# Kernel optimization log

Hardware: AMD Instinct MI355X
Metric: run time of the kernel (lower is better)

## Reference

```python
import jax, jax.numpy as jnp
import numpy as np

N_E = 8192
E_DIM = 512
BETA = 0.25


def setup_inputs() -> dict:
    key = jax.random.key(0)
    k1, k2, k3, k4 = jax.random.split(key, 4)
    x = jax.random.normal(k1, (32, 512, E_DIM), dtype=jnp.float32)
    label = jax.random.randint(k2, (32, 512), 0, 100, dtype=jnp.int64)
    idx = jax.random.randint(k3, (32, 512), 0, 512, dtype=jnp.int64)
    # codebook initialized uniform(-1/n_e, 1/n_e) as in the torch module
    W = jax.random.uniform(k4, (N_E, E_DIM), dtype=jnp.float32,
                           minval=-1.0 / N_E, maxval=1.0 / N_E)
    return {"x": x, "label": label, "idx": idx, "W": W}


def reference(x, label, idx, W):
    # label/idx are unused in the forward math (mirrors the torch module)
    latent = x.reshape(-1, E_DIM)                        # [N, e_dim]
    # squared euclidean distances: ||z||^2 + ||c||^2 - 2 z c^T
    d = (jnp.sum(latent ** 2, axis=1, keepdims=True)
         + jnp.sum(W ** 2, axis=1)[None, :]
         - 2.0 * jnp.matmul(latent, W.T))                # [N, n_e]
    indices = jnp.argmin(d, axis=-1)                     # [N]
    x_q = W[indices].reshape(x.shape)                    # gather + reshape
    commitment_loss = jnp.mean((jax.lax.stop_gradient(x_q) - x) ** 2)
    loss = BETA * commitment_loss
    # straight-through estimator
    x_q = x + jax.lax.stop_gradient(x_q - x)
    indices = indices.reshape(x.shape[:-1])
    return x_q, loss, indices
```

## Files before the change

### kernel.cpp

```cpp
#include <hip/hip_runtime.h>
#include <cstdint>
#include <cstddef>

#define EDIM  512
#define NROWS 16384
#define NE    8192
#define XQSZ  (NROWS * EDIM)
#define NTILE 64
#define K3    1536

#define OFF_PART  0
#define OFF_Z     16384
#define OFF_C2    81920
#define OFF_KEYS  114688
#define OFF_TMIN  245760
#define OFF_CNT   4440064
#define OFF_LIST  4441088
#define OFF_XE    8635392
#define OFF_WE    58967040

typedef __attribute__((ext_vector_type(8)))  short          short8;
typedef __attribute__((ext_vector_type(16))) float          f32x16;
typedef __attribute__((ext_vector_type(4)))  unsigned short u16x4;

__global__ void k_rownorm(const float* __restrict__ in, float* __restrict__ out, int nrows) {
#pragma clang fp contract(off)
    int row = blockIdx.x * blockDim.x + threadIdx.x;
    if (row >= nrows) return;
    const float* p = in + (size_t)row * EDIM;
    float S[4];
#pragma unroll
    for (int b = 0; b < 4; ++b) {
        const float* q = p + b * 128;
        float r[8];
#pragma unroll
        for (int j = 0; j < 8; ++j) { float v = q[j]; r[j] = v * v; }
        for (int i = 8; i < 128; i += 8) {
#pragma unroll
            for (int j = 0; j < 8; ++j) { float v = q[i + j]; r[j] = r[j] + v * v; }
        }
        S[b] = ((r[0] + r[1]) + (r[2] + r[3])) + ((r[4] + r[5]) + (r[6] + r[7]));
    }
    out[row] = (S[0] + S[1]) + (S[2] + S[3]);
}

__device__ __forceinline__ unsigned short f2bf(float f) {
    unsigned u = __float_as_uint(f);
    return (unsigned short)((u + 0x7FFFu + ((u >> 16) & 1u)) >> 16);
}
__device__ __forceinline__ float bf2f(unsigned short h) {
    return __uint_as_float(((unsigned)h) << 16);
}

__global__ __launch_bounds__(256) void k_split3(const float* __restrict__ in,
        unsigned short* __restrict__ outp, int nrows) {
    int e = blockIdx.x * 256 + threadIdx.x;
    int row = e >> 7;
    int d0  = (e & 127) << 2;
    if (row >= nrows) return;
    float4 v = *(const float4*)(in + (size_t)row * EDIM + d0);
    float vv[4] = {v.x, v.y, v.z, v.w};
    u16x4 H, M, L;
#pragma unroll
    for (int i = 0; i < 4; ++i) {
        float f = vv[i];
        unsigned short h = f2bf(f);
        float r1 = f - bf2f(h);
        unsigned short m = f2bf(r1);
        float r2 = r1 - bf2f(m);
        L[i] = f2bf(r2); H[i] = h; M[i] = m;
    }
    unsigned short* o = outp + (size_t)row * K3 + d0;
    *(u16x4*)(o) = H; *(u16x4*)(o + EDIM) = M; *(u16x4*)(o + 2 * EDIM) = L;
}

__device__ __forceinline__ void gld16(const void* g, void* l) {
    __builtin_amdgcn_global_load_lds((const __attribute__((address_space(1))) void*)g,
                                     (__attribute__((address_space(3))) void*)l, 16, 0, 0);
}

#define GBM 128
#define GBN 128
#define GBK 64

__global__ __launch_bounds__(256) void k_argmin_hi(
        const unsigned short* __restrict__ Xe, const unsigned short* __restrict__ We,
        const float* __restrict__ c2, unsigned* __restrict__ tmin) {
    __shared__ __align__(16) unsigned short At[GBM * GBK];
    __shared__ __align__(16) unsigned short Bt[GBN * GBK];
    __shared__ unsigned smin[GBM];

    const int tid = threadIdx.x;
    const int lane = tid & 63, wid = tid >> 6;
    const int wr = wid >> 1, wc = wid & 1;

    const int bid = blockIdx.x;
    const int swz = (bid & 7) * 1024 + (bid >> 3);
    const int rowtile = swz & 127, codetile = swz >> 7;
    const int row0 = rowtile * GBM, code0 = codetile * GBN;

    if (tid < GBM) smin[tid] = 0xFFFFFFFFu;

    f32x16 acc[2][2];
#pragma unroll
    for (int i = 0; i < 2; ++i)
#pragma unroll
        for (int j = 0; j < 2; ++j)
#pragma unroll
            for (int r = 0; r < 16; ++r) acc[i][j][r] = 0.0f;

    size_t ga[4], gb[4];
#pragma unroll
    for (int i = 0; i < 4; ++i) {
        int chunk = i * 256 + tid;
        int row   = chunk >> 3;
        int kcs   = (chunk & 7) ^ (row & 7);
        ga[i] = (size_t)(row0 + row) * K3 + kcs * 8;
        gb[i] = (size_t)(code0 + row) * K3 + kcs * 8;
    }

    const int ra0 = wr * 64 + (lane & 31);
    const int rb0 = wc * 64 + (lane & 31);
    const int kh  = lane >> 5;
    const int sa  = ra0 & 7, sb = rb0 & 7;

    for (int kt = 0; kt < EDIM / GBK; ++kt) {
        const size_t ko = (size_t)kt * GBK;
#pragma unroll
        for (int i = 0; i < 4; ++i) {
            gld16(Xe + ga[i] + ko, (char*)At + i * 4096 + wid * 1024);
            gld16(We + gb[i] + ko, (char*)Bt + i * 4096 + wid * 1024);
        }
        __syncthreads();
#pragma unroll
        for (int ks = 0; ks < 4; ++ks) {
            const int ch = ks * 2 + kh;
            short8 a0 = *(const short8*)((const char*)At + ra0 * 128        + ((ch ^ sa) * 16));
            short8 a1 = *(const short8*)((const char*)At + (ra0 + 32) * 128 + ((ch ^ sa) * 16));
            short8 b0 = *(const short8*)((const char*)Bt + rb0 * 128        + ((ch ^ sb) * 16));
            short8 b1 = *(const short8*)((const char*)Bt + (rb0 + 32) * 128 + ((ch ^ sb) * 16));
            acc[0][0] = __builtin_amdgcn_mfma_f32_32x32x16_bf16(a0, b0, acc[0][0], 0, 0, 0);
            acc[0][1] = __builtin_amdgcn_mfma_f32_32x32x16_bf16(a0, b1, acc[0][1], 0, 0, 0);
            acc[1][0] = __builtin_amdgcn_mfma_f32_32x32x16_bf16(a1, b0, acc[1][0], 0, 0, 0);
            acc[1][1] = __builtin_amdgcn_mfma_f32_32x32x16_bf16(a1, b1, acc[1][1], 0, 0, 0);
        }
        __syncthreads();
    }

    const int j0 = code0 + wc * 64 + (lane & 31);
    const float c20 = c2[j0], c21 = c2[j0 + 32];
#pragma unroll
    for (int mi = 0; mi < 2; ++mi) {
#pragma unroll
        for (int reg = 0; reg < 16; ++reg) {
            const int rl = wr * 64 + mi * 32 + (reg & 3) + 8 * (reg >> 2) + 4 * kh;
            const float d0 = (4.0f + c20) - 2.0f * acc[mi][0][reg];
            const float d1 = (4.0f + c21) - 2.0f * acc[mi][1][reg];
            unsigned u0 = __float_as_uint(d0), u1 = __float_as_uint(d1);
            unsigned u = u0 < u1 ? u0 : u1;
#pragma unroll
            for (int m = 1; m <= 16; m <<= 1) {
                unsigned o = __shfl_xor(u, m, 64);
                if (o < u) u = o;
            }
            if ((lane & 31) == 0) atomicMin(&smin[rl], u);
        }
    }
    __syncthreads();
    if (tid < GBM) tmin[codetile * NROWS + row0 + tid] = smin[tid];
}

__global__ __launch_bounds__(256) void k_select(
        const unsigned* __restrict__ tmin, const float* __restrict__ Z,
        int* __restrict__ cnt, int* __restrict__ list) {
    const int row = blockIdx.x * 256 + threadIdx.x;
    unsigned mn = 0xFFFFFFFFu;
    for (int t = 0; t < NTILE; ++t) {
        unsigned v = tmin[t * NROWS + row];
        if (v < mn) mn = v;
    }
    const float margin = 4.35e-5f * sqrtf(Z[row]) + 1.7e-4f;
    const float thr = __uint_as_float(mn) + margin;
    for (int t = 0; t < NTILE; ++t) {
        if (__uint_as_float(tmin[t * NROWS + row]) <= thr) {
            int p = atomicAdd(&cnt[t], 1);
            list[t * NROWS + p] = row;
        }
    }
}

__global__ __launch_bounds__(256) void k_rescore_mfma(
        const unsigned short* __restrict__ Xe, const unsigned short* __restrict__ We,
        const float* __restrict__ Z, const float* __restrict__ c2,
        const int* __restrict__ cnt, const int* __restrict__ list,
        unsigned long long* __restrict__ keys) {
    __shared__ __align__(16) unsigned short At[GBM * GBK];
    __shared__ __align__(16) unsigned short Bt[GBN * GBK];
    __shared__ int rl_s[GBM];
    __shared__ float Zs[GBM];

    const int tile = blockIdx.x;
    const int n = cnt[tile];
    if (n == 0) return;
    const int* rows = list + tile * NROWS;
    const int tid = threadIdx.x;
    const int lane = tid & 63, wid = tid >> 6;
    const int wr = wid >> 1, wc = wid & 1;
    const int code0 = tile * 128;

    const int ra0 = wr * 64 + (lane & 31);
    const int rb0 = wc * 64 + (lane & 31);
    const int kh  = lane >> 5;
    const int sa  = ra0 & 7, sb = rb0 & 7;
    const int j0 = code0 + wc * 64 + (lane & 31);
    const float c20 = c2[j0], c21 = c2[j0 + 32];

    for (int chk = (int)blockIdx.y; chk * GBM < n; chk += 16) {
        __syncthreads();
        if (tid < GBM) {
            int ri = chk * GBM + tid;
            int r = rows[ri < n ? ri : 0];
            rl_s[tid] = r;
            Zs[tid] = Z[r];
        }
        __syncthreads();

        size_t aoff[4], boff[4];
#pragma unroll
        for (int i = 0; i < 4; ++i) {
            int chunk = i * 256 + tid;
            int row   = chunk >> 3;
            int kcs   = (chunk & 7) ^ (row & 7);
            aoff[i] = (size_t)rl_s[row] * K3 + kcs * 8;
            boff[i] = (size_t)(code0 + row) * K3 + kcs * 8;
        }

        f32x16 acc[2][2];
#pragma unroll
        for (int i = 0; i < 2; ++i)
#pragma unroll
            for (int j = 0; j < 2; ++j)
#pragma unroll
                for (int r = 0; r < 16; ++r) acc[i][j][r] = 0.0f;

#pragma unroll
        for (int bt = 0; bt < 6; ++bt) {
            const int ao = (bt == 1 || bt == 2) ? EDIM : (bt == 4 ? 2 * EDIM : 0);
            const int bo = (bt == 0 || bt == 2) ? EDIM : (bt == 3 ? 2 * EDIM : 0);
            for (int kc = 0; kc < 8; ++kc) {
                const int ko = ao + kc * GBK;
                const int kob = bo + kc * GBK;
#pragma unroll
                for (int i = 0; i < 4; ++i) {
                    gld16(Xe + aoff[i] + ko,  (char*)At + i * 4096 + wid * 1024);
                    gld16(We + boff[i] + kob, (char*)Bt + i * 4096 + wid * 1024);
                }
                __syncthreads();
#pragma unroll
                for (int ks = 0; ks < 4; ++ks) {
                    const int ch = ks * 2 + kh;
                    short8 a0 = *(const short8*)((const char*)At + ra0 * 128        + ((ch ^ sa) * 16));
                    short8 a1 = *(const short8*)((const char*)At + (ra0 + 32) * 128 + ((ch ^ sa) * 16));
                    short8 b0 = *(const short8*)((const char*)Bt + rb0 * 128        + ((ch ^ sb) * 16));
                    short8 b1 = *(const short8*)((const char*)Bt + (rb0 + 32) * 128 + ((ch ^ sb) * 16));
                    acc[0][0] = __builtin_amdgcn_mfma_f32_32x32x16_bf16(a0, b0, acc[0][0], 0, 0, 0);
                    acc[0][1] = __builtin_amdgcn_mfma_f32_32x32x16_bf16(a0, b1, acc[0][1], 0, 0, 0);
                    acc[1][0] = __builtin_amdgcn_mfma_f32_32x32x16_bf16(a1, b0, acc[1][0], 0, 0, 0);
                    acc[1][1] = __builtin_amdgcn_mfma_f32_32x32x16_bf16(a1, b1, acc[1][1], 0, 0, 0);
                }
                __syncthreads();
            }
        }

#pragma unroll
        for (int mi = 0; mi < 2; ++mi) {
#pragma unroll
            for (int reg = 0; reg < 16; ++reg) {
                const int rl = wr * 64 + mi * 32 + (reg & 3) + 8 * (reg >> 2) + 4 * kh;
                const float Zr = Zs[rl];
                const float d0 = (Zr + c20) - 2.0f * acc[mi][0][reg];
                const float d1 = (Zr + c21) - 2.0f * acc[mi][1][reg];
                unsigned long long k0 = (((unsigned long long)__float_as_uint(d0)) << 13) | (unsigned)j0;
                unsigned long long k1 = (((unsigned long long)__float_as_uint(d1)) << 13) | (unsigned)(j0 + 32);
                unsigned long long k = k0 < k1 ? k0 : k1;
#pragma unroll
                for (int m = 1; m <= 16; m <<= 1) {
                    unsigned long long o = __shfl_xor(k, m, 64);
                    if (o < k) k = o;
                }
                if ((lane & 31) == 0) atomicMin(&keys[rl_s[rl]], k);
            }
        }
    }
}

__global__ __launch_bounds__(256) void k_gather(
        const float* __restrict__ x, const float* __restrict__ W,
        const unsigned long long* __restrict__ keys,
        float* __restrict__ out, double* __restrict__ part) {
    const int tid = threadIdx.x;
    const int row = blockIdx.x * 8 + (tid >> 5);
    const int c = tid & 31;
    const int idx = (int)(keys[row] & 0x1FFFull);

    const float* wrow = W + (size_t)idx * EDIM;
    const float* xrow = x + (size_t)row * EDIM;
    float* orow = out + (size_t)row * EDIM;

    double lsum = 0.0;
#pragma unroll
    for (int v = 0; v < 4; ++v) {
        const int d = c * 4 + v * 128;
        float4 xv = *(const float4*)(xrow + d);
        float4 wv = *(const float4*)(wrow + d);
        float t0 = wv.x - xv.x, t1 = wv.y - xv.y, t2 = wv.z - xv.z, t3 = wv.w - xv.w;
        float4 ov = { xv.x + t0, xv.y + t1, xv.z + t2, xv.w + t3 };
        *(float4*)(orow + d) = ov;
        lsum += (double)t0 * t0 + (double)t1 * t1 + (double)t2 * t2 + (double)t3 * t3;
    }
    if (c == 0) out[XQSZ + 1 + row] = (float)idx;

#pragma unroll
    for (int off = 32; off > 0; off >>= 1) lsum += __shfl_down(lsum, off, 64);
    __shared__ double pb[4];
    if ((tid & 63) == 0) pb[tid >> 6] = lsum;
    __syncthreads();
    if (tid == 0) part[blockIdx.x] = pb[0] + pb[1] + pb[2] + pb[3];
}

__global__ __launch_bounds__(256) void k_finalize(float* __restrict__ out,
        const double* __restrict__ part) {
    const int tid = threadIdx.x;
    double s = 0.0;
    for (int i = tid; i < 2048; i += 256) s += part[i];
#pragma unroll
    for (int off = 32; off > 0; off >>= 1) s += __shfl_down(s, off, 64);
    __shared__ double pb[4];
    if ((tid & 63) == 0) pb[tid >> 6] = s;
    __syncthreads();
    if (tid == 0) out[XQSZ] = (float)(0.25 * (pb[0] + pb[1] + pb[2] + pb[3]) / (double)XQSZ);
}

extern "C" void kernel_launch(void* const* d_in, const int* in_sizes, int n_in,
                              void* d_out, int out_size, void* d_ws, size_t ws_size,
                              hipStream_t stream) {
    const float* x = (const float*)d_in[0];
    const float* W = (const float*)d_in[3];
    float* out = (float*)d_out;
    char* ws = (char*)d_ws;

    double* part = (double*)(ws + OFF_PART);
    float* Z    = (float*)(ws + OFF_Z);
    float* c2   = (float*)(ws + OFF_C2);
    unsigned long long* keys = (unsigned long long*)(ws + OFF_KEYS);
    unsigned* tmin = (unsigned*)(ws + OFF_TMIN);
    int* cnt  = (int*)(ws + OFF_CNT);
    int* list = (int*)(ws + OFF_LIST);
    unsigned short* Xe = (unsigned short*)(ws + OFF_XE);
    unsigned short* We = (unsigned short*)(ws + OFF_WE);

    hipMemsetAsync(keys, 0xFF, NROWS * sizeof(unsigned long long), stream);
    hipMemsetAsync(cnt, 0, NTILE * sizeof(int), stream);
    k_rownorm<<<NROWS / 256, 256, 0, stream>>>(x, Z, NROWS);
    k_rownorm<<<NE / 256, 256, 0, stream>>>(W, c2, NE);
    k_split3<<<(NROWS * 128) / 256, 256, 0, stream>>>(x, Xe, NROWS);
    k_split3<<<(NE * 128) / 256, 256, 0, stream>>>(W, We, NE);
    k_argmin_hi<<<(NROWS / GBM) * (NE / GBN), 256, 0, stream>>>(Xe, We, c2, tmin);
    k_select<<<NROWS / 256, 256, 0, stream>>>(tmin, Z, cnt, list);
    k_rescore_mfma<<<dim3(NTILE, 16), 256, 0, stream>>>(Xe, We, Z, c2, cnt, list, keys);
    k_gather<<<NROWS / 8, 256, 0, stream>>>(x, W, keys, out, part);
    k_finalize<<<1, 256, 0, stream>>>(out, part);
}
```

Before: 583.1 us.

## Transpose MFMA operands so argmin reduces within lanes instead of shuffles

```diff
diff --git a/kernel.cpp b/kernel.cpp
--- a/kernel.cpp
+++ b/kernel.cpp
@@ -89,6 +89,7 @@
     __shared__ __align__(16) unsigned short At[GBM * GBK];
     __shared__ __align__(16) unsigned short Bt[GBN * GBK];
     __shared__ unsigned smin[GBM];
+    __shared__ float cs[GBN];
 
     const int tid = threadIdx.x;
     const int lane = tid & 63, wid = tid >> 6;
@@ -100,6 +101,7 @@
     const int row0 = rowtile * GBM, code0 = codetile * GBN;
 
     if (tid < GBM) smin[tid] = 0xFFFFFFFFu;
+    if (tid < GBN) cs[tid] = 4.0f + c2[code0 + tid];
 
     f32x16 acc[2][2];
 #pragma unroll
@@ -119,10 +121,10 @@
         gb[i] = (size_t)(code0 + row) * K3 + kcs * 8;
     }
 
-    const int ra0 = wr * 64 + (lane & 31);
-    const int rb0 = wc * 64 + (lane & 31);
+    const int cb0 = wr * 64 + (lane & 31);
+    const int xa0 = wc * 64 + (lane & 31);
     const int kh  = lane >> 5;
-    const int sa  = ra0 & 7, sb = rb0 & 7;
+    const int sb  = cb0 & 7, sa = xa0 & 7;
 
     for (int kt = 0; kt < EDIM / GBK; ++kt) {
         const size_t ko = (size_t)kt * GBK;
@@ -135,36 +137,35 @@
 #pragma unroll
         for (int ks = 0; ks < 4; ++ks) {
             const int ch = ks * 2 + kh;
-            short8 a0 = *(const short8*)((const char*)At + ra0 * 128        + ((ch ^ sa) * 16));
-            short8 a1 = *(const short8*)((const char*)At + (ra0 + 32) * 128 + ((ch ^ sa) * 16));
-            short8 b0 = *(const short8*)((const char*)Bt + rb0 * 128        + ((ch ^ sb) * 16));
-            short8 b1 = *(const short8*)((const char*)Bt + (rb0 + 32) * 128 + ((ch ^ sb) * 16));
-            acc[0][0] = __builtin_amdgcn_mfma_f32_32x32x16_bf16(a0, b0, acc[0][0], 0, 0, 0);
-            acc[0][1] = __builtin_amdgcn_mfma_f32_32x32x16_bf16(a0, b1, acc[0][1], 0, 0, 0);
-            acc[1][0] = __builtin_amdgcn_mfma_f32_32x32x16_bf16(a1, b0, acc[1][0], 0, 0, 0);
-            acc[1][1] = __builtin_amdgcn_mfma_f32_32x32x16_bf16(a1, b1, acc[1][1], 0, 0, 0);
+            short8 c0 = *(const short8*)((const char*)Bt + cb0 * 128        + ((ch ^ sb) * 16));
+            short8 c1 = *(const short8*)((const char*)Bt + (cb0 + 32) * 128 + ((ch ^ sb) * 16));
+            short8 x0 = *(const short8*)((const char*)At + xa0 * 128        + ((ch ^ sa) * 16));
+            short8 x1 = *(const short8*)((const char*)At + (xa0 + 32) * 128 + ((ch ^ sa) * 16));
+            acc[0][0] = __builtin_amdgcn_mfma_f32_32x32x16_bf16(c0, x0, acc[0][0], 0, 0, 0);
+            acc[0][1] = __builtin_amdgcn_mfma_f32_32x32x16_bf16(c0, x1, acc[0][1], 0, 0, 0);
+            acc[1][0] = __builtin_amdgcn_mfma_f32_32x32x16_bf16(c1, x0, acc[1][0], 0, 0, 0);
+            acc[1][1] = __builtin_amdgcn_mfma_f32_32x32x16_bf16(c1, x1, acc[1][1], 0, 0, 0);
         }
         __syncthreads();
     }
 
-    const int j0 = code0 + wc * 64 + (lane & 31);
-    const float c20 = c2[j0], c21 = c2[j0 + 32];
-#pragma unroll
-    for (int mi = 0; mi < 2; ++mi) {
-#pragma unroll
-        for (int reg = 0; reg < 16; ++reg) {
-            const int rl = wr * 64 + mi * 32 + (reg & 3) + 8 * (reg >> 2) + 4 * kh;
-            const float d0 = (4.0f + c20) - 2.0f * acc[mi][0][reg];
-            const float d1 = (4.0f + c21) - 2.0f * acc[mi][1][reg];
-            unsigned u0 = __float_as_uint(d0), u1 = __float_as_uint(d1);
-            unsigned u = u0 < u1 ? u0 : u1;
-#pragma unroll
-            for (int m = 1; m <= 16; m <<= 1) {
-                unsigned o = __shfl_xor(u, m, 64);
-                if (o < u) u = o;
+    const int kh4 = kh * 4;
+#pragma unroll
+    for (int nj = 0; nj < 2; ++nj) {
+        float dmin = 3.4e38f;
+#pragma unroll
+        for (int mi = 0; mi < 2; ++mi) {
+#pragma unroll
+            for (int q = 0; q < 4; ++q) {
+                const float4 cq = *(const float4*)&cs[wr * 64 + mi * 32 + q * 8 + kh4];
+                dmin = fminf(dmin, fmaf(-2.0f, acc[mi][nj][q * 4 + 0], cq.x));
+                dmin = fminf(dmin, fmaf(-2.0f, acc[mi][nj][q * 4 + 1], cq.y));
+                dmin = fminf(dmin, fmaf(-2.0f, acc[mi][nj][q * 4 + 2], cq.z));
+                dmin = fminf(dmin, fmaf(-2.0f, acc[mi][nj][q * 4 + 3], cq.w));
             }
-            if ((lane & 31) == 0) atomicMin(&smin[rl], u);
-        }
+        }
+        const int xr = wc * 64 + nj * 32 + (lane & 31);
+        atomicMin(&smin[xr], __float_as_uint(dmin));
     }
     __syncthreads();
     if (tid < GBM) tmin[codetile * NROWS + row0 + tid] = smin[tid];
@@ -198,6 +199,7 @@
     __shared__ __align__(16) unsigned short Bt[GBN * GBK];
     __shared__ int rl_s[GBM];
     __shared__ float Zs[GBM];
+    __shared__ float cs2[GBN];
 
     const int tile = blockIdx.x;
     const int n = cnt[tile];
@@ -208,12 +210,13 @@
     const int wr = wid >> 1, wc = wid & 1;
     const int code0 = tile * 128;
 
-    const int ra0 = wr * 64 + (lane & 31);
-    const int rb0 = wc * 64 + (lane & 31);
+    if (tid < GBN) cs2[tid] = c2[code0 + tid];
+
+    const int cb0 = wr * 64 + (lane & 31);
+    const int xa0 = wc * 64 + (lane & 31);
     const int kh  = lane >> 5;
-    const int sa  = ra0 & 7, sb = rb0 & 7;
-    const int j0 = code0 + wc * 64 + (lane & 31);
-    const float c20 = c2[j0], c21 = c2[j0 + 32];
+    const int kh4 = kh * 4;
+    const int sb  = cb0 & 7, sa = xa0 & 7;
 
     for (int chk = (int)blockIdx.y; chk * GBM < n; chk += 16) {
         __syncthreads();
@@ -259,37 +262,43 @@
 #pragma unroll
                 for (int ks = 0; ks < 4; ++ks) {
                     const int ch = ks * 2 + kh;
-                    short8 a0 = *(const short8*)((const char*)At + ra0 * 128        + ((ch ^ sa) * 16));
-                    short8 a1 = *(const short8*)((const char*)At + (ra0 + 32) * 128 + ((ch ^ sa) * 16));
-                    short8 b0 = *(const short8*)((const char*)Bt + rb0 * 128        + ((ch ^ sb) * 16));
-                    short8 b1 = *(const short8*)((const char*)Bt + (rb0 + 32) * 128 + ((ch ^ sb) * 16));
-                    acc[0][0] = __builtin_amdgcn_mfma_f32_32x32x16_bf16(a0, b0, acc[0][0], 0, 0, 0);
-                    acc[0][1] = __builtin_amdgcn_mfma_f32_32x32x16_bf16(a0, b1, acc[0][1], 0, 0, 0);
-                    acc[1][0] = __builtin_amdgcn_mfma_f32_32x32x16_bf16(a1, b0, acc[1][0], 0, 0, 0);
-                    acc[1][1] = __builtin_amdgcn_mfma_f32_32x32x16_bf16(a1, b1, acc[1][1], 0, 0, 0);
+                    short8 c0 = *(const short8*)((const char*)Bt + cb0 * 128        + ((ch ^ sb) * 16));
+                    short8 c1 = *(const short8*)((const char*)Bt + (cb0 + 32) * 128 + ((ch ^ sb) * 16));
+                    short8 x0 = *(const short8*)((const char*)At + xa0 * 128        + ((ch ^ sa) * 16));
+                    short8 x1 = *(const short8*)((const char*)At + (xa0 + 32) * 128 + ((ch ^ sa) * 16));
+                    acc[0][0] = __builtin_amdgcn_mfma_f32_32x32x16_bf16(c0, x0, acc[0][0], 0, 0, 0);
+                    acc[0][1] = __builtin_amdgcn_mfma_f32_32x32x16_bf16(c0, x1, acc[0][1], 0, 0, 0);
+                    acc[1][0] = __builtin_amdgcn_mfma_f32_32x32x16_bf16(c1, x0, acc[1][0], 0, 0, 0);
+                    acc[1][1] = __builtin_amdgcn_mfma_f32_32x32x16_bf16(c1, x1, acc[1][1], 0, 0, 0);
                 }
                 __syncthreads();
             }
         }
 
 #pragma unroll
-        for (int mi = 0; mi < 2; ++mi) {
-#pragma unroll
-            for (int reg = 0; reg < 16; ++reg) {
-                const int rl = wr * 64 + mi * 32 + (reg & 3) + 8 * (reg >> 2) + 4 * kh;
-                const float Zr = Zs[rl];
-                const float d0 = (Zr + c20) - 2.0f * acc[mi][0][reg];
-                const float d1 = (Zr + c21) - 2.0f * acc[mi][1][reg];
-                unsigned long long k0 = (((unsigned long long)__float_as_uint(d0)) << 13) | (unsigned)j0;
-                unsigned long long k1 = (((unsigned long long)__float_as_uint(d1)) << 13) | (unsigned)(j0 + 32);
-                unsigned long long k = k0 < k1 ? k0 : k1;
-#pragma unroll
-                for (int m = 1; m <= 16; m <<= 1) {
-                    unsigned long long o = __shfl_xor(k, m, 64);
-                    if (o < k) k = o;
+        for (int nj = 0; nj < 2; ++nj) {
+            const int xr = wc * 64 + nj * 32 + (lane & 31);
+            const float Zr = Zs[xr];
+            float dm = 3.4e38f; int jm = 0;
+#pragma unroll
+            for (int mi = 0; mi < 2; ++mi) {
+#pragma unroll
+                for (int q = 0; q < 4; ++q) {
+                    const float4 cq = *(const float4*)&cs2[wr * 64 + mi * 32 + q * 8 + kh4];
+                    const int jb = code0 + wr * 64 + mi * 32 + q * 8 + kh4;
+                    { const float d = (Zr + cq.x) - 2.0f * acc[mi][nj][q * 4 + 0];
+                      if (d < dm) { dm = d; jm = jb + 0; } }
+                    { const float d = (Zr + cq.y) - 2.0f * acc[mi][nj][q * 4 + 1];
+                      if (d < dm) { dm = d; jm = jb + 1; } }
+                    { const float d = (Zr + cq.z) - 2.0f * acc[mi][nj][q * 4 + 2];
+                      if (d < dm) { dm = d; jm = jb + 2; } }
+                    { const float d = (Zr + cq.w) - 2.0f * acc[mi][nj][q * 4 + 3];
+                      if (d < dm) { dm = d; jm = jb + 3; } }
                 }
-                if ((lane & 31) == 0) atomicMin(&keys[rl_s[rl]], k);
             }
+            const unsigned long long k =
+                (((unsigned long long)__float_as_uint(dm)) << 13) | (unsigned)jm;
+            atomicMin(&keys[rl_s[xr]], k);
         }
     }
 }
```

New measurement: 535.6 us. -8.1%, faster.
